# Performance work log

Measured on AMD Instinct MI355X. Metric: run time of the kernel, lower is better.

The kernel has to match this reference:

```python
import jax, jax.numpy as jnp
import numpy as np

N = 50000          # nodes
E = 800000         # edges (before self-loops)
F_IN, F_HID, F_OUT = 128, 64, 64
NEG_SLOPE_ATT = 0.2   # GATConv internal leaky_relu
NEG_SLOPE_ACT = 0.01  # F.leaky_relu default between layers


def setup_inputs() -> dict:
    key = jax.random.key(0)
    ks = jax.random.split(key, 16)

    def glorot(k, shape):
        fan = float(sum(shape)) if len(shape) > 1 else float(shape[0])
        return jax.random.normal(k, shape, jnp.float32) * (2.0 / fan) ** 0.5

    return {
        "x": jax.random.normal(ks[0], (N, F_IN), jnp.float32),
        "edge_index": jax.random.randint(ks[1], (2, E), 0, N, dtype=jnp.int64),
        "W1": glorot(ks[2], (F_IN, F_HID)),
        "a_src1": glorot(ks[3], (F_HID,)),
        "a_dst1": glorot(ks[4], (F_HID,)),
        "b1": jnp.zeros((F_HID,), jnp.float32),
        "W2": glorot(ks[5], (F_HID, F_HID)),
        "a_src2": glorot(ks[6], (F_HID,)),
        "a_dst2": glorot(ks[7], (F_HID,)),
        "b2": jnp.zeros((F_HID,), jnp.float32),
        "W3": glorot(ks[8], (F_HID, F_OUT)),
        "a_src3": glorot(ks[9], (F_OUT,)),
        "a_dst3": glorot(ks[10], (F_OUT,)),
        "b3": jnp.zeros((F_OUT,), jnp.float32),
    }


def gat_conv(h, src, dst, W, a_src, a_dst, b):
    # Single-head PyG GATConv: project, per-edge scores, segment softmax over dst, scatter-add.
    z = h @ W                              # [N, C]
    e_src = z @ a_src                      # [N]
    e_dst = z @ a_dst                      # [N]
    e = jax.nn.leaky_relu(e_src[src] + e_dst[dst], NEG_SLOPE_ATT)  # [E']
    m = jax.ops.segment_max(e, dst, num_segments=N)
    ex = jnp.exp(e - m[dst])
    denom = jax.ops.segment_sum(ex, dst, num_segments=N)
    alpha = ex / (denom[dst] + 1e-16)      # segment softmax (PyG adds 1e-16)
    out = jax.ops.segment_sum(alpha[:, None] * z[src], dst, num_segments=N) + b
    return out, alpha


def reference(x, edge_index, W1, a_src1, a_dst1, b1, W2, a_src2, a_dst2, b2, W3, a_src3, a_dst3, b3):
    # add_self_loops=True (GATConv default): append (i, i) for every node
    loops = jnp.arange(N, dtype=edge_index.dtype)
    ei = jnp.concatenate([edge_index, jnp.stack([loops, loops])], axis=1)  # [2, E+N]
    src, dst = ei[0], ei[1]

    h = x
    alpha = None
    for (W, asr, ads, b) in ((W1, a_src1, a_dst1, b1),
                             (W2, a_src2, a_dst2, b2),
                             (W3, a_src3, a_dst3, b3)):
        h, alpha = gat_conv(h, src, dst, W, asr, ads, b)
        h = jax.nn.leaky_relu(h, NEG_SLOPE_ACT)
    return (h, ei, alpha)
```

## Files before the change

kernel.cpp:

```cpp
#include <hip/hip_runtime.h>
#include <hip/hip_bf16.h>
#include <hip/hip_fp8.h>

#define NN 50000
#define EE 800000
#define E2 850000
#define F_IN 128
#define F_HID 64
#define NCHUNK ((NN + 255) / 256)
#define NTILE  ((NN + 63) / 64)
#define SLICES 512
#define SCHUNK ((E2 + SLICES - 1) / SLICES)

__device__ __forceinline__ unsigned char f32_to_fp8(float x) {
    __hip_fp8_e4m3 t(x);
    return t.__x;
}
__device__ __forceinline__ float fp8_to_f32(unsigned char b) {
    __hip_fp8_e4m3 t; t.__x = b;
    return (float)t;
}
__device__ __forceinline__ float readlane_f(float v, int l) {
    return __uint_as_float(__builtin_amdgcn_readlane(__float_as_uint(v), l));
}

__global__ __launch_bounds__(256) void hist_ei_kernel(const int* __restrict__ ei,
                                                      int* __restrict__ deg,
                                                      float* __restrict__ ei_out) {
    int e = blockIdx.x * 256 + threadIdx.x;
    if (e >= E2) return;
    int s, d;
    if (e < EE) { s = ei[e]; d = ei[EE + e]; }
    else        { s = d = e - EE; }
    atomicAdd(&deg[d], 1);
    ei_out[e]      = (float)s;
    ei_out[E2 + e] = (float)d;
}

__global__ __launch_bounds__(256) void scan_part1(const int* __restrict__ deg,
                                                  int* __restrict__ csum) {
    int i = blockIdx.x * 256 + threadIdx.x;
    int v = (i < NN) ? deg[i] : 0;
#pragma unroll
    for (int d = 32; d; d >>= 1) v += __shfl_xor(v, d);
    __shared__ int ws[4];
    if ((threadIdx.x & 63) == 0) ws[threadIdx.x >> 6] = v;
    __syncthreads();
    if (threadIdx.x == 0) csum[blockIdx.x] = ws[0] + ws[1] + ws[2] + ws[3];
}

__global__ __launch_bounds__(256) void scan_part2(int* __restrict__ csum) {
    __shared__ int sd[256];
    int t = threadIdx.x;
    int v = (t < NCHUNK) ? csum[t] : 0;
    sd[t] = v;
    __syncthreads();
    for (int off = 1; off < 256; off <<= 1) {
        int o = (t >= off) ? sd[t - off] : 0;
        __syncthreads();
        sd[t] += o;
        __syncthreads();
    }
    if (t < NCHUNK) csum[t] = sd[t] - v;
}

__global__ __launch_bounds__(256) void scan_part3(const int* __restrict__ deg,
                                                  const int* __restrict__ csum,
                                                  int* __restrict__ offs,
                                                  int* __restrict__ cursor) {
    __shared__ int sd[256];
    int t = threadIdx.x;
    int i = blockIdx.x * 256 + t;
    int v = (i < NN) ? deg[i] : 0;
    sd[t] = v;
    __syncthreads();
    for (int off = 1; off < 256; off <<= 1) {
        int o = (t >= off) ? sd[t - off] : 0;
        __syncthreads();
        sd[t] += o;
        __syncthreads();
    }
    if (i < NN) {
        int ex = sd[t] - v + csum[blockIdx.x];
        offs[i] = ex;
        cursor[i] = ex;
    }
}

__global__ __launch_bounds__(256) void scatter_kernel(const int* __restrict__ ei,
                                                      int* __restrict__ cursor,
                                                      int* __restrict__ src_sorted) {
    int g = blockIdx.x & 7;
    int slice = blockIdx.x >> 3;
    int begin = slice * SCHUNK;
    int end = begin + SCHUNK; if (end > E2) end = E2;
    for (int e = begin + threadIdx.x; e < end; e += 256) {
        int s, d;
        if (e < EE) { s = ei[e]; d = ei[EE + e]; }
        else        { s = d = e - EE; }
        int bucket = (d * 8) / NN;
        if (bucket == g) {
            int pos = atomicAdd(&cursor[d], 1);
            src_sorted[pos] = s;
        }
    }
}

template <int K>
__global__ __launch_bounds__(256) void gemm_tile(const float* __restrict__ h,
                                                 const float* __restrict__ W,
                                                 const float* __restrict__ a_src,
                                                 const float* __restrict__ a_dst,
                                                 unsigned char* __restrict__ z8,
                                                 float* __restrict__ es,
                                                 float* __restrict__ ed) {
    constexpr int LDA = K + 4;
    __shared__ float Alds[64 * LDA];
    __shared__ float Blds[K * 64];

    int tid = threadIdx.x;
    int base = blockIdx.x * 64;

    {
        constexpr int F4R = K / 4;
        for (int t = tid; t < 64 * F4R; t += 256) {
            int r = t / F4R;
            int c4 = t % F4R;
            int gr = base + r;
            if (gr >= NN) gr = NN - 1;
            float4 v = *(const float4*)(h + (size_t)gr * K + c4 * 4);
            *(float4*)(&Alds[r * LDA + c4 * 4]) = v;
        }
    }
    for (int t = tid; t < K * 16; t += 256) {
        float4 v = *(const float4*)(W + t * 4);
        *(float4*)(&Blds[t * 4]) = v;
    }
    __syncthreads();

    int tx = tid & 15;
    int ty = tid >> 4;

    float acc[4][4] = {};
#pragma unroll 4
    for (int k = 0; k < K; k += 4) {
        float4 a[4], b[4];
#pragma unroll
        for (int i = 0; i < 4; ++i)
            a[i] = *(const float4*)(&Alds[(4 * ty + i) * LDA + k]);
#pragma unroll
        for (int kk = 0; kk < 4; ++kk)
            b[kk] = *(const float4*)(&Blds[(k + kk) * 64 + 4 * tx]);
#pragma unroll
        for (int i = 0; i < 4; ++i) {
            acc[i][0] = fmaf(a[i].x, b[0].x, acc[i][0]);
            acc[i][1] = fmaf(a[i].x, b[0].y, acc[i][1]);
            acc[i][2] = fmaf(a[i].x, b[0].z, acc[i][2]);
            acc[i][3] = fmaf(a[i].x, b[0].w, acc[i][3]);
            acc[i][0] = fmaf(a[i].y, b[1].x, acc[i][0]);
            acc[i][1] = fmaf(a[i].y, b[1].y, acc[i][1]);
            acc[i][2] = fmaf(a[i].y, b[1].z, acc[i][2]);
            acc[i][3] = fmaf(a[i].y, b[1].w, acc[i][3]);
            acc[i][0] = fmaf(a[i].z, b[2].x, acc[i][0]);
            acc[i][1] = fmaf(a[i].z, b[2].y, acc[i][1]);
            acc[i][2] = fmaf(a[i].z, b[2].z, acc[i][2]);
            acc[i][3] = fmaf(a[i].z, b[2].w, acc[i][3]);
            acc[i][0] = fmaf(a[i].w, b[3].x, acc[i][0]);
            acc[i][1] = fmaf(a[i].w, b[3].y, acc[i][1]);
            acc[i][2] = fmaf(a[i].w, b[3].z, acc[i][2]);
            acc[i][3] = fmaf(a[i].w, b[3].w, acc[i][3]);
        }
    }

    float4 as4 = *(const float4*)(a_src + 4 * tx);
    float4 ad4 = *(const float4*)(a_dst + 4 * tx);
    float ps[4], pd[4];
#pragma unroll
    for (int i = 0; i < 4; ++i) {
        int gr = base + 4 * ty + i;
        if (gr < NN) {
            unsigned int pk = (unsigned int)f32_to_fp8(acc[i][0])
                            | ((unsigned int)f32_to_fp8(acc[i][1]) << 8)
                            | ((unsigned int)f32_to_fp8(acc[i][2]) << 16)
                            | ((unsigned int)f32_to_fp8(acc[i][3]) << 24);
            *(unsigned int*)(&z8[(size_t)gr * 64 + 4 * tx]) = pk;
        }
        ps[i] = acc[i][0] * as4.x + acc[i][1] * as4.y + acc[i][2] * as4.z + acc[i][3] * as4.w;
        pd[i] = acc[i][0] * ad4.x + acc[i][1] * ad4.y + acc[i][2] * ad4.z + acc[i][3] * ad4.w;
    }
#pragma unroll
    for (int d = 1; d < 16; d <<= 1) {
#pragma unroll
        for (int i = 0; i < 4; ++i) {
            ps[i] += __shfl_xor(ps[i], d);
            pd[i] += __shfl_xor(pd[i], d);
        }
    }
    if (tx == 0) {
#pragma unroll
        for (int i = 0; i < 4; ++i) {
            int gr = base + 4 * ty + i;
            if (gr < NN) { es[gr] = ps[i]; ed[gr] = pd[i]; }
        }
    }
}

__global__ __launch_bounds__(256) void aggregate(const int* __restrict__ offs,
                                                 const int* __restrict__ deg,
                                                 const int* __restrict__ src_sorted,
                                                 const float* __restrict__ es,
                                                 const float* __restrict__ ed,
                                                 const unsigned char* __restrict__ z8,
                                                 const float* __restrict__ bias,
                                                 float* __restrict__ hout,
                                                 float* __restrict__ denom_out) {
    int tid = threadIdx.x;
    int lane = tid & 63;
    int wv = tid >> 6;
    int n = blockIdx.x * 4 + wv;
    if (n >= NN) return;
    n = __builtin_amdgcn_readfirstlane(n);

    int off = offs[n];
    int dg = deg[n];
    float edn = ed[n];

    float dsum = 0.f;
    float a0 = 0.f, a1 = 0.f, a2 = 0.f, a3 = 0.f;

    for (int b0 = 0; b0 < dg; b0 += 64) {
        int bl = dg - b0; if (bl > 64) bl = 64;
        int idx = off + b0 + ((lane < bl) ? lane : 0);
        int sv = src_sorted[idx];
        float e = es[sv] + edn;
        e = (e > 0.f) ? e : 0.2f * e;
        float w = (lane < bl) ? __expf(e) : 0.f;
        dsum += w;

        int j = 0;
        for (; j + 4 <= bl; j += 4) {
            int   s0 = __builtin_amdgcn_readlane(sv, j);
            int   s1 = __builtin_amdgcn_readlane(sv, j + 1);
            int   s2 = __builtin_amdgcn_readlane(sv, j + 2);
            int   s3 = __builtin_amdgcn_readlane(sv, j + 3);
            float w0 = readlane_f(w, j);
            float w1 = readlane_f(w, j + 1);
            float w2 = readlane_f(w, j + 2);
            float w3 = readlane_f(w, j + 3);
            a0 = fmaf(w0, fp8_to_f32(z8[(size_t)s0 * 64 + lane]), a0);
            a1 = fmaf(w1, fp8_to_f32(z8[(size_t)s1 * 64 + lane]), a1);
            a2 = fmaf(w2, fp8_to_f32(z8[(size_t)s2 * 64 + lane]), a2);
            a3 = fmaf(w3, fp8_to_f32(z8[(size_t)s3 * 64 + lane]), a3);
        }
        for (; j < bl; ++j) {
            int   s0 = __builtin_amdgcn_readlane(sv, j);
            float w0 = readlane_f(w, j);
            a0 = fmaf(w0, fp8_to_f32(z8[(size_t)s0 * 64 + lane]), a0);
        }
    }

#pragma unroll
    for (int d = 32; d; d >>= 1) dsum += __shfl_xor(dsum, d);

    float acc = (a0 + a1) + (a2 + a3);
    float inv = 1.f / (dsum + 1e-16f);
    float o = acc * inv + bias[lane];
    o = (o > 0.f) ? o : 0.01f * o;

    hout[(size_t)n * 64 + lane] = o;
    if (lane == 0) denom_out[n] = dsum;
}

__global__ __launch_bounds__(256) void alpha_kernel(const int* __restrict__ ei,
                                                    const float* __restrict__ es,
                                                    const float* __restrict__ ed,
                                                    const float* __restrict__ denom,
                                                    float* __restrict__ alpha_out) {
    int e = blockIdx.x * 256 + threadIdx.x;
    if (e >= E2) return;
    int s, d;
    if (e < EE) { s = ei[e]; d = ei[EE + e]; }
    else        { s = d = e - EE; }
    float x = es[s] + ed[d];
    x = (x > 0.f) ? x : 0.2f * x;
    alpha_out[e] = __expf(x) / (denom[d] + 1e-16f);
}

extern "C" void kernel_launch(void* const* d_in, const int* in_sizes, int n_in,
                              void* d_out, int out_size, void* d_ws, size_t ws_size,
                              hipStream_t stream) {
    const float* x   = (const float*)d_in[0];
    const int*   ei  = (const int*)d_in[1];
    const float* W1  = (const float*)d_in[2];
    const float* as1 = (const float*)d_in[3];
    const float* ad1 = (const float*)d_in[4];
    const float* b1  = (const float*)d_in[5];
    const float* W2  = (const float*)d_in[6];
    const float* as2 = (const float*)d_in[7];
    const float* ad2 = (const float*)d_in[8];
    const float* b2  = (const float*)d_in[9];
    const float* W3  = (const float*)d_in[10];
    const float* as3 = (const float*)d_in[11];
    const float* ad3 = (const float*)d_in[12];
    const float* b3  = (const float*)d_in[13];

    float* out       = (float*)d_out;
    float* h_out     = out;
    float* ei_out    = out + (size_t)NN * 64;
    float* alpha_out = ei_out + 2 * (size_t)E2;

    char* w = (char*)d_ws;
    auto carve = [&](size_t bytes) {
        void* p = (void*)w;
        w += (bytes + 255) & ~size_t(255);
        return p;
    };
    float* h1  = (float*)carve((size_t)NN * 64 * 4);
    float* h2  = (float*)carve((size_t)NN * 64 * 4);
    unsigned char* z8 = (unsigned char*)carve((size_t)NN * 64);
    float* es  = (float*)carve((size_t)NN * 4);
    float* ed  = (float*)carve((size_t)NN * 4);
    float* denom = (float*)carve((size_t)NN * 4);
    int* deg        = (int*)carve((size_t)NN * 4);
    int* offs       = (int*)carve((size_t)NN * 4);
    int* cursor     = (int*)carve((size_t)NN * 4);
    int* csum       = (int*)carve((size_t)NCHUNK * 4);
    int* src_sorted = (int*)carve((size_t)E2 * 4);

    const int EB = (E2 + 255) / 256;
    const int NB = (NN + 3) / 4;

    hipMemsetAsync(deg, 0, (size_t)NN * 4, stream);
    hist_ei_kernel<<<EB, 256, 0, stream>>>(ei, deg, ei_out);
    scan_part1<<<NCHUNK, 256, 0, stream>>>(deg, csum);
    scan_part2<<<1, 256, 0, stream>>>(csum);
    scan_part3<<<NCHUNK, 256, 0, stream>>>(deg, csum, offs, cursor);
    scatter_kernel<<<SLICES * 8, 256, 0, stream>>>(ei, cursor, src_sorted);

    gemm_tile<F_IN><<<NTILE, 256, 0, stream>>>(x, W1, as1, ad1, z8, es, ed);
    aggregate<<<NB, 256, 0, stream>>>(offs, deg, src_sorted, es, ed, z8, b1, h1, denom);
    gemm_tile<F_HID><<<NTILE, 256, 0, stream>>>(h1, W2, as2, ad2, z8, es, ed);
    aggregate<<<NB, 256, 0, stream>>>(offs, deg, src_sorted, es, ed, z8, b2, h2, denom);
    gemm_tile<F_HID><<<NTILE, 256, 0, stream>>>(h2, W3, as3, ad3, z8, es, ed);
    aggregate<<<NB, 256, 0, stream>>>(offs, deg, src_sorted, es, ed, z8, b3, h_out, denom);
    alpha_kernel<<<EB, 256, 0, stream>>>(ei, es, ed, denom, alpha_out);
}
```

Before: 326.6 us.

## Persistent aggregate waves with next-node prefetch; fuse scan passes via last-block ticket

The aggregate kernel becomes grid-strided, with 2048 blocks whose waves loop over nodes. Each wave prefetches the next node's offset, degree, dst score and first source-index batch while it processes the current node. The inner gather loop is unrolled to 8 independent accumulators so more fp8 row loads are in flight at once. The first two scan kernels are merged into one, where the last block to arrive (found with an atomic ticket) does the chunk-prefix scan, saving a launch at the cost of atomics and fences.

```diff
diff --git a/kernel.cpp b/kernel.cpp
--- a/kernel.cpp
+++ b/kernel.cpp
@@ -11,6 +11,7 @@
 #define NTILE  ((NN + 63) / 64)
 #define SLICES 512
 #define SCHUNK ((E2 + SLICES - 1) / SLICES)
+#define AGGB 2048
 
 __device__ __forceinline__ unsigned char f32_to_fp8(float x) {
     __hip_fp8_e4m3 t(x);
@@ -37,8 +38,9 @@
     ei_out[E2 + e] = (float)d;
 }
 
-__global__ __launch_bounds__(256) void scan_part1(const int* __restrict__ deg,
-                                                  int* __restrict__ csum) {
+__global__ __launch_bounds__(256) void scan_part12(const int* __restrict__ deg,
+                                                   int* __restrict__ csum,
+                                                   int* __restrict__ ticket) {
     int i = blockIdx.x * 256 + threadIdx.x;
     int v = (i < NN) ? deg[i] : 0;
 #pragma unroll
@@ -46,22 +48,28 @@
     __shared__ int ws[4];
     if ((threadIdx.x & 63) == 0) ws[threadIdx.x >> 6] = v;
     __syncthreads();
-    if (threadIdx.x == 0) csum[blockIdx.x] = ws[0] + ws[1] + ws[2] + ws[3];
-}
-
-__global__ __launch_bounds__(256) void scan_part2(int* __restrict__ csum) {
-    __shared__ int sd[256];
-    int t = threadIdx.x;
-    int v = (t < NCHUNK) ? csum[t] : 0;
-    sd[t] = v;
+    __shared__ int isLast;
+    if (threadIdx.x == 0) {
+        atomicExch(&csum[blockIdx.x], ws[0] + ws[1] + ws[2] + ws[3]);
+        __threadfence();
+        isLast = (atomicAdd(ticket, 1) == gridDim.x - 1) ? 1 : 0;
+    }
     __syncthreads();
-    for (int off = 1; off < 256; off <<= 1) {
-        int o = (t >= off) ? sd[t - off] : 0;
+    if (isLast) {
+        __threadfence();
+        __shared__ int sd[256];
+        int t = threadIdx.x;
+        int v2 = (t < NCHUNK) ? atomicAdd(&csum[t], 0) : 0;
+        sd[t] = v2;
         __syncthreads();
-        sd[t] += o;
-        __syncthreads();
-    }
-    if (t < NCHUNK) csum[t] = sd[t] - v;
+        for (int off = 1; off < 256; off <<= 1) {
+            int o = (t >= off) ? sd[t - off] : 0;
+            __syncthreads();
+            sd[t] += o;
+            __syncthreads();
+        }
+        if (t < NCHUNK) atomicExch(&csum[t], sd[t] - v2);
+    }
 }
 
 __global__ __launch_bounds__(256) void scan_part3(const int* __restrict__ deg,
@@ -216,59 +224,96 @@
                                                  float* __restrict__ denom_out) {
     int tid = threadIdx.x;
     int lane = tid & 63;
-    int wv = tid >> 6;
-    int n = blockIdx.x * 4 + wv;
+    int wave = blockIdx.x * 4 + (tid >> 6);
+    const int NW = AGGB * 4;
+    float bi = bias[lane];
+
+    int n = wave;
     if (n >= NN) return;
     n = __builtin_amdgcn_readfirstlane(n);
-
     int off = offs[n];
     int dg = deg[n];
     float edn = ed[n];
-
-    float dsum = 0.f;
-    float a0 = 0.f, a1 = 0.f, a2 = 0.f, a3 = 0.f;
-
-    for (int b0 = 0; b0 < dg; b0 += 64) {
-        int bl = dg - b0; if (bl > 64) bl = 64;
-        int idx = off + b0 + ((lane < bl) ? lane : 0);
-        int sv = src_sorted[idx];
-        float e = es[sv] + edn;
-        e = (e > 0.f) ? e : 0.2f * e;
-        float w = (lane < bl) ? __expf(e) : 0.f;
-        dsum += w;
-
-        int j = 0;
-        for (; j + 4 <= bl; j += 4) {
-            int   s0 = __builtin_amdgcn_readlane(sv, j);
-            int   s1 = __builtin_amdgcn_readlane(sv, j + 1);
-            int   s2 = __builtin_amdgcn_readlane(sv, j + 2);
-            int   s3 = __builtin_amdgcn_readlane(sv, j + 3);
-            float w0 = readlane_f(w, j);
-            float w1 = readlane_f(w, j + 1);
-            float w2 = readlane_f(w, j + 2);
-            float w3 = readlane_f(w, j + 3);
-            a0 = fmaf(w0, fp8_to_f32(z8[(size_t)s0 * 64 + lane]), a0);
-            a1 = fmaf(w1, fp8_to_f32(z8[(size_t)s1 * 64 + lane]), a1);
-            a2 = fmaf(w2, fp8_to_f32(z8[(size_t)s2 * 64 + lane]), a2);
-            a3 = fmaf(w3, fp8_to_f32(z8[(size_t)s3 * 64 + lane]), a3);
-        }
-        for (; j < bl; ++j) {
-            int   s0 = __builtin_amdgcn_readlane(sv, j);
-            float w0 = readlane_f(w, j);
-            a0 = fmaf(w0, fp8_to_f32(z8[(size_t)s0 * 64 + lane]), a0);
-        }
-    }
-
-#pragma unroll
-    for (int d = 32; d; d >>= 1) dsum += __shfl_xor(dsum, d);
-
-    float acc = (a0 + a1) + (a2 + a3);
-    float inv = 1.f / (dsum + 1e-16f);
-    float o = acc * inv + bias[lane];
-    o = (o > 0.f) ? o : 0.01f * o;
-
-    hout[(size_t)n * 64 + lane] = o;
-    if (lane == 0) denom_out[n] = dsum;
+    int sv = src_sorted[off + ((lane < dg) ? lane : 0)];
+
+    while (true) {
+        int n2 = n + NW;
+        bool more = (n2 < NN);
+        int off2 = 0, dg2 = 0; float edn2 = 0.f;
+        if (more) {
+            n2 = __builtin_amdgcn_readfirstlane(n2);
+            off2 = offs[n2]; dg2 = deg[n2]; edn2 = ed[n2];
+        }
+
+        float dsum = 0.f;
+        float a0 = 0.f, a1 = 0.f, a2 = 0.f, a3 = 0.f;
+        float a4 = 0.f, a5 = 0.f, a6 = 0.f, a7 = 0.f;
+        for (int b0 = 0; b0 < dg; b0 += 64) {
+            int bl = dg - b0; if (bl > 64) bl = 64;
+            int svb = (b0 == 0) ? sv
+                                : src_sorted[off + b0 + ((lane < bl) ? lane : 0)];
+            float e = es[svb] + edn;
+            e = (e > 0.f) ? e : 0.2f * e;
+            float w = (lane < bl) ? __expf(e) : 0.f;
+            dsum += w;
+
+            int j = 0;
+            for (; j + 8 <= bl; j += 8) {
+                int   s0 = __builtin_amdgcn_readlane(svb, j);
+                int   s1 = __builtin_amdgcn_readlane(svb, j + 1);
+                int   s2 = __builtin_amdgcn_readlane(svb, j + 2);
+                int   s3 = __builtin_amdgcn_readlane(svb, j + 3);
+                int   s4 = __builtin_amdgcn_readlane(svb, j + 4);
+                int   s5 = __builtin_amdgcn_readlane(svb, j + 5);
+                int   s6 = __builtin_amdgcn_readlane(svb, j + 6);
+                int   s7 = __builtin_amdgcn_readlane(svb, j + 7);
+                float w0 = readlane_f(w, j),     w1 = readlane_f(w, j + 1);
+                float w2 = readlane_f(w, j + 2), w3 = readlane_f(w, j + 3);
+                float w4 = readlane_f(w, j + 4), w5 = readlane_f(w, j + 5);
+                float w6 = readlane_f(w, j + 6), w7 = readlane_f(w, j + 7);
+                a0 = fmaf(w0, fp8_to_f32(z8[(size_t)s0 * 64 + lane]), a0);
+                a1 = fmaf(w1, fp8_to_f32(z8[(size_t)s1 * 64 + lane]), a1);
+                a2 = fmaf(w2, fp8_to_f32(z8[(size_t)s2 * 64 + lane]), a2);
+                a3 = fmaf(w3, fp8_to_f32(z8[(size_t)s3 * 64 + lane]), a3);
+                a4 = fmaf(w4, fp8_to_f32(z8[(size_t)s4 * 64 + lane]), a4);
+                a5 = fmaf(w5, fp8_to_f32(z8[(size_t)s5 * 64 + lane]), a5);
+                a6 = fmaf(w6, fp8_to_f32(z8[(size_t)s6 * 64 + lane]), a6);
+                a7 = fmaf(w7, fp8_to_f32(z8[(size_t)s7 * 64 + lane]), a7);
+            }
+            for (; j + 4 <= bl; j += 4) {
+                int   s0 = __builtin_amdgcn_readlane(svb, j);
+                int   s1 = __builtin_amdgcn_readlane(svb, j + 1);
+                int   s2 = __builtin_amdgcn_readlane(svb, j + 2);
+                int   s3 = __builtin_amdgcn_readlane(svb, j + 3);
+                float w0 = readlane_f(w, j),     w1 = readlane_f(w, j + 1);
+                float w2 = readlane_f(w, j + 2), w3 = readlane_f(w, j + 3);
+                a0 = fmaf(w0, fp8_to_f32(z8[(size_t)s0 * 64 + lane]), a0);
+                a1 = fmaf(w1, fp8_to_f32(z8[(size_t)s1 * 64 + lane]), a1);
+                a2 = fmaf(w2, fp8_to_f32(z8[(size_t)s2 * 64 + lane]), a2);
+                a3 = fmaf(w3, fp8_to_f32(z8[(size_t)s3 * 64 + lane]), a3);
+            }
+            for (; j < bl; ++j) {
+                int   s0 = __builtin_amdgcn_readlane(svb, j);
+                float w0 = readlane_f(w, j);
+                a0 = fmaf(w0, fp8_to_f32(z8[(size_t)s0 * 64 + lane]), a0);
+            }
+        }
+
+        int sv2 = 0;
+        if (more) sv2 = src_sorted[off2 + ((lane < dg2) ? lane : 0)];
+
+#pragma unroll
+        for (int d = 32; d; d >>= 1) dsum += __shfl_xor(dsum, d);
+        float acc = ((a0 + a1) + (a2 + a3)) + ((a4 + a5) + (a6 + a7));
+        float inv = 1.f / (dsum + 1e-16f);
+        float o = acc * inv + bi;
+        o = (o > 0.f) ? o : 0.01f * o;
+        hout[(size_t)n * 64 + lane] = o;
+        if (lane == 0) denom_out[n] = dsum;
+
+        if (!more) break;
+        n = n2; off = off2; dg = dg2; edn = edn2; sv = sv2;
+    }
 }
 
 __global__ __launch_bounds__(256) void alpha_kernel(const int* __restrict__ ei,
@@ -321,27 +366,26 @@
     float* es  = (float*)carve((size_t)NN * 4);
     float* ed  = (float*)carve((size_t)NN * 4);
     float* denom = (float*)carve((size_t)NN * 4);
-    int* deg        = (int*)carve((size_t)NN * 4);
+    int* deg        = (int*)carve(((size_t)NN + 64) * 4);
+    int* ticket     = deg + NN;
     int* offs       = (int*)carve((size_t)NN * 4);
     int* cursor     = (int*)carve((size_t)NN * 4);
     int* csum       = (int*)carve((size_t)NCHUNK * 4);
     int* src_sorted = (int*)carve((size_t)E2 * 4);
 
     const int EB = (E2 + 255) / 256;
-    const int NB = (NN + 3) / 4;
-
-    hipMemsetAsync(deg, 0, (size_t)NN * 4, stream);
+
+    hipMemsetAsync(deg, 0, ((size_t)NN + 64) * 4, stream);
     hist_ei_kernel<<<EB, 256, 0, stream>>>(ei, deg, ei_out);
-    scan_part1<<<NCHUNK, 256, 0, stream>>>(deg, csum);
-    scan_part2<<<1, 256, 0, stream>>>(csum);
+    scan_part12<<<NCHUNK, 256, 0, stream>>>(deg, csum, ticket);
     scan_part3<<<NCHUNK, 256, 0, stream>>>(deg, csum, offs, cursor);
     scatter_kernel<<<SLICES * 8, 256, 0, stream>>>(ei, cursor, src_sorted);
 
     gemm_tile<F_IN><<<NTILE, 256, 0, stream>>>(x, W1, as1, ad1, z8, es, ed);
-    aggregate<<<NB, 256, 0, stream>>>(offs, deg, src_sorted, es, ed, z8, b1, h1, denom);
+    aggregate<<<AGGB, 256, 0, stream>>>(offs, deg, src_sorted, es, ed, z8, b1, h1, denom);
     gemm_tile<F_HID><<<NTILE, 256, 0, stream>>>(h1, W2, as2, ad2, z8, es, ed);
-    aggregate<<<NB, 256, 0, stream>>>(offs, deg, src_sorted, es, ed, z8, b2, h2, denom);
+    aggregate<<<AGGB, 256, 0, stream>>>(offs, deg, src_sorted, es, ed, z8, b2, h2, denom);
     gemm_tile<F_HID><<<NTILE, 256, 0, stream>>>(h2, W3, as3, ad3, z8, es, ed);
-    aggregate<<<NB, 256, 0, stream>>>(offs, deg, src_sorted, es, ed, z8, b3, h_out, denom);
+    aggregate<<<AGGB, 256, 0, stream>>>(offs, deg, src_sorted, es, ed, z8, b3, h_out, denom);
     alpha_kernel<<<EB, 256, 0, stream>>>(ei, es, ed, denom, alpha_out);
 }
```

New measurement: 316.9 us. -3.0%, faster.
